# Kernel tuning notes

Measured on AMD Instinct MI355X. Metric: run time of the kernel, lower is better.

Reference implementation:

```python
import jax, jax.numpy as jnp
import numpy as np

WS = (7, 7, 7)          # window size (d, h, w)
N = WS[0] * WS[1] * WS[2]   # 343 tokens per window
C = 96                  # embed_dim
H = 24                  # num_heads  (constraint: embed_dim = 4 * num_heads)
HD = C // H             # head_dim = 4
B = 32                  # number of windows in the batch
SCALE = HD ** -0.5
EPS = 1e-5


def _relative_position_index():
    # identical to the torch buffer construction in MSA_block.__init__
    coords = np.stack(np.meshgrid(np.arange(WS[0]), np.arange(WS[1]), np.arange(WS[2]), indexing='ij'))
    flat = coords.reshape(3, -1)                       # [3, N]
    rel = flat[:, :, None] - flat[:, None, :]          # [3, N, N]
    rel = rel.transpose(1, 2, 0).astype(np.int64)      # [N, N, 3]
    rel[..., 0] += WS[0] - 1
    rel[..., 1] += WS[1] - 1
    rel[..., 2] += WS[2] - 1
    rel[..., 0] *= (2 * WS[1] - 1) * (2 * WS[2] - 1)
    rel[..., 1] *= 2 * WS[2] - 1
    return rel.sum(-1).astype(np.int32)                # [N, N]


def setup_inputs() -> dict:
    key = jax.random.key(0)
    ks = jax.random.split(key, 9)
    table_size = (2 * WS[0] - 1) * (2 * WS[1] - 1) * (2 * WS[2] - 1)   # 2197
    return {
        'x1': jax.random.normal(ks[0], (B, N, C), jnp.float32),
        'x2': jax.random.normal(ks[1], (B, N, C), jnp.float32),
        'qkv_w': jax.random.normal(ks[2], (3 * C, C), jnp.float32) * 0.02,
        'qkv_b': jax.random.normal(ks[3], (3 * C,), jnp.float32) * 0.02,
        'proj_w': jax.random.normal(ks[4], (C, C), jnp.float32) * 0.02,
        'proj_b': jax.random.normal(ks[5], (C,), jnp.float32) * 0.02,
        'rpb_table': jax.random.normal(ks[6], (table_size, H), jnp.float32) * 0.02,
        'fuse_w': jax.random.normal(ks[7], (H, 2 * H), jnp.float32) * 0.1,   # Conv2d 1x1: [out_c=H, in_c=2H]
        'fuse_b': jax.random.normal(ks[8], (H,), jnp.float32) * 0.02,
        'rel_index': jnp.asarray(_relative_position_index()),
    }


def _qkv(x, qkv_w, qkv_b):
    b, n, c = x.shape
    qkv = (x @ qkv_w.T + qkv_b).reshape(b, n, 3, H, HD)
    qkv = jnp.transpose(qkv, (2, 0, 3, 1, 4))          # [3, b, H, n, hd]
    return qkv[0], qkv[1], qkv[2]


def reference(x1, x2, qkv_w, qkv_b, proj_w, proj_b, rpb_table, fuse_w, fuse_b, rel_index):
    b, n, c = x1.shape
    q1, k1, v1 = _qkv(x1, qkv_w, qkv_b)
    q2, k2, v2 = _qkv(x2, qkv_w, qkv_b)
    attn1 = jnp.einsum('bhqd,bhkd->bhqk', q1 * SCALE, k1)
    attn2 = jnp.einsum('bhqd,bhkd->bhqk', q2 * SCALE, k2)

    # fuse: 1x1 Conv2d over channel dim (2H -> H) + InstanceNorm2d + ReLU + Sigmoid
    v = jnp.concatenate((v1, v2), axis=1)              # [b, 2H, n, hd]
    v = jnp.einsum('bcnd,oc->bond', v, fuse_w) + fuse_b[None, :, None, None]
    mean = v.mean(axis=(2, 3), keepdims=True)
    var = v.var(axis=(2, 3), keepdims=True)
    v = (v - mean) * jax.lax.rsqrt(var + EPS)
    v = jax.nn.sigmoid(jax.nn.relu(v))                 # [b, H, n, hd]

    # gathered relative-position bias: [n, n, H] -> [H, n, n]
    bias = rpb_table[rel_index.reshape(-1)].reshape(n, n, H)
    bias = jnp.transpose(bias, (2, 0, 1))

    attn = jax.nn.softmax(attn1 + attn2 + bias[None], axis=-1)
    out = jnp.einsum('bhqk,bhkd->bhqd', attn, v)       # [b, H, n, hd]
    out = jnp.transpose(out, (0, 2, 1, 3)).reshape(b, n, c)
    return out @ proj_w.T + proj_b
```

## Files before the change

### kernel.cpp

```cpp
#include <hip/hip_runtime.h>
#include <hip/hip_bf16.h>

#define N_TOK 343
#define N_PAD 344
#define BT_J 352
#define C_DIM 96
#define H_HEADS 24
#define HD 4
#define B_WIN 32
#define LOG2E 1.4426950408889634f
#define SCALE_Q (0.5f * LOG2E)
#define EPS_IN 1e-5f
#define CH_STR (HD * N_PAD)
#define F4_STR (N_PAD)
#define AP ((size_t)B_WIN * H_HEADS * CH_STR)
#define BT_ELEMS ((size_t)H_HEADS * BT_J * N_PAD)
#define BT_FLOAT_SPACE ((BT_ELEMS + 1) / 2)
#define PS_HALF ((size_t)B_WIN * H_HEADS * N_PAD)

typedef float v2f __attribute__((ext_vector_type(2)));
#define FMA2(a, b, c) __builtin_elementwise_fma(a, b, c)

__device__ __forceinline__ unsigned short f2bf(float v) {
    unsigned u = __float_as_uint(v);
    u += 0x7FFFu + ((u >> 16) & 1u);
    return (unsigned short)(u >> 16);
}

__global__ __launch_bounds__(192) void prep_kernel(const float* __restrict__ x1,
                                                   const float* __restrict__ x2,
                                                   const float* __restrict__ w,
                                                   const float* __restrict__ bqkv,
                                                   const float* __restrict__ rpb,
                                                   const int* __restrict__ rel,
                                                   float* __restrict__ ws,
                                                   unsigned short* __restrict__ bT) {
    __shared__ float smem[12704];
    const int bid = blockIdx.x, tid = threadIdx.x;
    if (bid < 2112) {
        const int r0t = bid % 11;
        const int rest = bid / 11;
        const int sy = rest % 6, b = rest / 6;
        const int s = sy >> 1, src = sy & 1;
        const int r0 = r0t * 32;
        const int rows = min(32, N_TOK - r0);
        float* xs = smem;
        float* wt = smem + 3104;
        for (int e = tid; e < 96 * 96; e += 192) {
            int j = e / 96, k = e - j * 96;
            wt[k * 100 + j] = w[s * 96 * 96 + e];
        }
        const float* xp = (src == 0 ? x1 : x2) + ((size_t)b * N_TOK + r0) * C_DIM;
        for (int e = tid; e < rows * 96; e += 192) {
            int r = e / 96, k = e - r * 96;
            xs[r * 97 + k] = xp[e];
        }
        __syncthreads();
        const int rg = tid & 7, og = tid >> 3;
        const int oc0 = og * 4, rr = rg * 4;
        float acc[4][4];
        #pragma unroll
        for (int i = 0; i < 4; ++i) {
            float bv = bqkv[s * 96 + oc0 + i];
            #pragma unroll
            for (int j = 0; j < 4; ++j) acc[i][j] = bv;
        }
        for (int k = 0; k < 96; ++k) {
            float4 w4 = *(const float4*)&wt[k * 100 + oc0];
            float wv[4] = {w4.x, w4.y, w4.z, w4.w};
            float xv[4];
            #pragma unroll
            for (int j = 0; j < 4; ++j) xv[j] = xs[(rr + j) * 97 + k];
            #pragma unroll
            for (int i = 0; i < 4; ++i)
                #pragma unroll
                for (int j = 0; j < 4; ++j) acc[i][j] += xv[j] * wv[i];
        }
        const float scl = (s == 0) ? SCALE_Q : 1.0f;
        const int slot = (s == 0) ? (src ? 2 : 0) : (s == 1) ? (src ? 3 : 1) : (src ? 5 : 4);
        #pragma unroll
        for (int j = 0; j < 4; ++j) {
            int row = r0 + rr + j;
            if (row > N_TOK) continue;
            size_t base = (((size_t)b * H_HEADS + og) * N_PAD + row) * 4;
            float4 val = (row == N_TOK)
                ? make_float4(0.f, 0.f, 0.f, 0.f)
                : make_float4(acc[0][j] * scl, acc[1][j] * scl,
                              acc[2][j] * scl, acc[3][j] * scl);
            *(float4*)(ws + (size_t)slot * AP + base) = val;
        }
    } else {
        const int bid2 = bid - 2112;
        const int h = bid2 / 121;
        const int t = bid2 - h * 121;
        const int ti = t / 11, tj = t - ti * 11;
        const int i0 = ti * 32, j0 = tj * 32;
        float* tile = smem;
        for (int e = tid; e < 1024; e += 192) {
            int r = e >> 5, c = e & 31;
            int i = i0 + r, j = j0 + c;
            float v = -16384.f;
            if (i < N_TOK && j < N_TOK) v = rpb[rel[i * N_TOK + j] * H_HEADS + h] * LOG2E;
            tile[r * 33 + c] = v;
        }
        __syncthreads();
        for (int e = tid; e < 1024; e += 192) {
            int c = e >> 5, r = e & 31;
            int i = i0 + r, j = j0 + c;
            if (i < N_PAD)
                bT[((size_t)h * BT_J + j) * N_PAD + i] = f2bf(tile[r * 33 + c]);
        }
    }
}

__global__ __launch_bounds__(256) void fuse_kernel(const float* __restrict__ v1,
                                                   const float* __restrict__ v2,
                                                   const float* __restrict__ fw,
                                                   const float* __restrict__ fb,
                                                   float* __restrict__ vf) {
    const int o = blockIdx.x, b = blockIdx.y;
    __shared__ float4 ts4[343];
    __shared__ float red[32];
    __shared__ float fwl[48];
    if (threadIdx.x < 48) fwl[threadIdx.x] = fw[o * 48 + threadIdx.x];
    __syncthreads();
    const float bo = fb[o];
    const float4* p1 = (const float4*)(v1 + (size_t)b * H_HEADS * CH_STR);
    const float4* p2 = (const float4*)(v2 + (size_t)b * H_HEADS * CH_STR);
    float lsum = 0.f, lsq = 0.f;
    for (int e = threadIdx.x; e < 343; e += blockDim.x) {
        float4 acc = make_float4(bo, bo, bo, bo);
        #pragma unroll
        for (int c = 0; c < H_HEADS; ++c) {
            float4 u1 = p1[(size_t)c * F4_STR + e];
            float4 u2 = p2[(size_t)c * F4_STR + e];
            float w1 = fwl[c], w2 = fwl[24 + c];
            acc.x += w1 * u1.x + w2 * u2.x;
            acc.y += w1 * u1.y + w2 * u2.y;
            acc.z += w1 * u1.z + w2 * u2.z;
            acc.w += w1 * u1.w + w2 * u2.w;
        }
        ts4[e] = acc;
        lsum += acc.x + acc.y + acc.z + acc.w;
        lsq += acc.x * acc.x + acc.y * acc.y + acc.z * acc.z + acc.w * acc.w;
    }
    for (int off = 32; off; off >>= 1) {
        lsum += __shfl_xor(lsum, off);
        lsq  += __shfl_xor(lsq, off);
    }
    int wid = threadIdx.x >> 6, lane = threadIdx.x & 63;
    if (lane == 0) { red[wid] = lsum; red[8 + wid] = lsq; }
    __syncthreads();
    if (threadIdx.x == 0) {
        float su = red[0] + red[1] + red[2] + red[3];
        float q  = red[8] + red[9] + red[10] + red[11];
        float mean = su / (float)(N_TOK * HD);
        float var  = q / (float)(N_TOK * HD) - mean * mean;
        red[16] = mean;
        red[17] = rsqrtf(var + EPS_IN);
    }
    __syncthreads();
    const float mean = red[16], inv = red[17];
    float4* outp = (float4*)(vf + ((size_t)b * H_HEADS + o) * CH_STR);
    for (int e = threadIdx.x; e < 343; e += blockDim.x) {
        float4 x = ts4[e];
        float4 r;
        r.x = 1.f / (1.f + __expf(-fmaxf((x.x - mean) * inv, 0.f)));
        r.y = 1.f / (1.f + __expf(-fmaxf((x.y - mean) * inv, 0.f)));
        r.z = 1.f / (1.f + __expf(-fmaxf((x.z - mean) * inv, 0.f)));
        r.w = 1.f / (1.f + __expf(-fmaxf((x.w - mean) * inv, 0.f)));
        outp[e] = r;
    }
}

struct JBatch { unsigned bu[4]; float4 k1[4], k2[4], vv[4]; };

#define LOAD_BATCH(B_, j0_)                                                  \
    _Pragma("unroll")                                                        \
    for (int u = 0; u < 4; ++u) {                                            \
        B_.bu[u] = *(const unsigned*)(bP + (size_t)((j0_) + u) * N_PAD);     \
        B_.k1[u] = K1[(j0_) + u];                                            \
        B_.k2[u] = K2[(j0_) + u];                                            \
        B_.vv[u] = Vv[(j0_) + u];                                            \
    }

#define COMP_BATCH(B_)                                                       \
    _Pragma("unroll")                                                        \
    for (int u = 0; u < 4; ++u) {                                            \
        const float4 k1 = B_.k1[u], k2 = B_.k2[u], v = B_.vv[u];             \
        v2f s2 = {__uint_as_float(B_.bu[u] << 16),                           \
                  __uint_as_float(B_.bu[u] & 0xffff0000u)};                  \
        s2 = FMA2((v2f)(k1.x), q1p0, s2); s2 = FMA2((v2f)(k1.y), q1p1, s2);  \
        s2 = FMA2((v2f)(k1.z), q1p2, s2); s2 = FMA2((v2f)(k1.w), q1p3, s2);  \
        s2 = FMA2((v2f)(k2.x), q2p0, s2); s2 = FMA2((v2f)(k2.y), q2p1, s2);  \
        s2 = FMA2((v2f)(k2.z), q2p2, s2); s2 = FMA2((v2f)(k2.w), q2p3, s2);  \
        const v2f p2 = {exp2f(s2.x), exp2f(s2.y)};                           \
        sum2 += p2;                                                          \
        a0 = FMA2(p2, (v2f)(v.x), a0); a1 = FMA2(p2, (v2f)(v.y), a1);        \
        a2 = FMA2(p2, (v2f)(v.z), a2); a3 = FMA2(p2, (v2f)(v.w), a3);        \
    }

#define ATTN_SETUP                                                                 \
    const size_t off = ((size_t)b * H_HEADS + h) * CH_STR;                         \
    const float4* __restrict__ K1 = (const float4*)(ws + 1 * AP + off);            \
    const float4* __restrict__ K2 = (const float4*)(ws + 3 * AP + off);            \
    const float4* __restrict__ Vv = (const float4*)(vf + off);                     \
    const float*  __restrict__ Q1 = ws + 0 * AP + off;                             \
    const float*  __restrict__ Q2 = ws + 2 * AP + off;                             \
    const int rA = l * 2, rB = rA + 1;                                             \
    const float4 q1a = *(const float4*)&Q1[rA * 4];                                \
    const float4 q1b = *(const float4*)&Q1[rB * 4];                                \
    const float4 q2a = *(const float4*)&Q2[rA * 4];                                \
    const float4 q2b = *(const float4*)&Q2[rB * 4];                                \
    const v2f q1p0 = {q1a.x, q1b.x}, q1p1 = {q1a.y, q1b.y},                        \
              q1p2 = {q1a.z, q1b.z}, q1p3 = {q1a.w, q1b.w};                        \
    const v2f q2p0 = {q2a.x, q2b.x}, q2p1 = {q2a.y, q2b.y},                        \
              q2p2 = {q2a.z, q2b.z}, q2p3 = {q2a.w, q2b.w};                        \
    v2f sum2 = {0.f, 0.f};                                                         \
    v2f a0 = {0.f, 0.f}, a1 = {0.f, 0.f}, a2 = {0.f, 0.f}, a3 = {0.f, 0.f};

template <int NBATCH>
__global__ __launch_bounds__(192) void attn_part_t(const float* __restrict__ ws,
                                                   const unsigned short* __restrict__ bT,
                                                   const float* __restrict__ vf,
                                                   float* __restrict__ Pa,
                                                   float* __restrict__ Ps) {
    const int h = blockIdx.x, b = blockIdx.y, part = blockIdx.z;
    const int l = threadIdx.x;
    if (l >= 172) return;
    ATTN_SETUP
    const int j0h = part * (NBATCH * 8);
    const unsigned short* bP = bT + ((size_t)h * BT_J + j0h) * N_PAD + rA;
    K1 += j0h; K2 += j0h; Vv += j0h;
    JBatch A, B;
    LOAD_BATCH(A, 0)
    LOAD_BATCH(B, 4)
    #pragma unroll
    for (int t = 0; t < NBATCH; ++t) {
        const int jb = t * 8;
        COMP_BATCH(A)
        if (t < NBATCH - 1) { LOAD_BATCH(A, jb + 8) }
        COMP_BATCH(B)
        if (t < NBATCH - 1) { LOAD_BATCH(B, jb + 12) }
    }
    float* PaH = Pa + (size_t)part * AP;
    float* PsH = Ps + (size_t)part * PS_HALF;
    const size_t pi = ((size_t)b * H_HEADS + h) * N_PAD;
    *(float4*)(PaH + (pi + rA) * 4) = make_float4(a0.x, a1.x, a2.x, a3.x);
    *(float4*)(PaH + (pi + rB) * 4) = make_float4(a0.y, a1.y, a2.y, a3.y);
    PsH[pi + rA] = sum2.x;
    PsH[pi + rB] = sum2.y;
}

__global__ __launch_bounds__(192) void attn_full(const float* __restrict__ ws,
                                                 const unsigned short* __restrict__ bT,
                                                 const float* __restrict__ vf,
                                                 float* __restrict__ ao) {
    const int h = blockIdx.x, b = blockIdx.y;
    const int l = threadIdx.x;
    if (l >= 172) return;
    ATTN_SETUP
    const unsigned short* bP = bT + (size_t)h * BT_J * N_PAD + rA;
    JBatch A, B;
    LOAD_BATCH(A, 0)
    LOAD_BATCH(B, 4)
    #pragma unroll
    for (int t = 0; t < 43; ++t) {
        const int jb = t * 8;
        COMP_BATCH(A)
        if (t < 42) { LOAD_BATCH(A, jb + 8) }
        COMP_BATCH(B)
        if (t < 42) { LOAD_BATCH(B, jb + 12) }
    }
    {
        const float inv = 1.f / sum2.x;
        float* op = ao + ((size_t)b * N_TOK + rA) * C_DIM + h * HD;
        *(float4*)op = make_float4(a0.x * inv, a1.x * inv, a2.x * inv, a3.x * inv);
    }
    if (rB < N_TOK) {
        const float inv = 1.f / sum2.y;
        float* op = ao + ((size_t)b * N_TOK + rB) * C_DIM + h * HD;
        *(float4*)op = make_float4(a0.y * inv, a1.y * inv, a2.y * inv, a3.y * inv);
    }
}

__global__ __launch_bounds__(256) void attn_kernel_g(const float* __restrict__ ws,
                                                     const float* __restrict__ rpb,
                                                     const int* __restrict__ rel,
                                                     const float* __restrict__ vf,
                                                     float* __restrict__ ao) {
    const int h = blockIdx.x, b = blockIdx.y;
    __shared__ float k1s[BT_J * 4], k2s[BT_J * 4], vs[BT_J * 4];
    __shared__ float q1s[N_PAD * 4], q2s[N_PAD * 4];
    const size_t off = ((size_t)b * H_HEADS + h) * CH_STR;
    const float* Q1 = ws + 0 * AP + off;
    const float* K1 = ws + 1 * AP + off;
    const float* Q2 = ws + 2 * AP + off;
    const float* K2 = ws + 3 * AP + off;
    const float* V  = vf + off;
    const int tid = threadIdx.x;
    for (int e = tid; e < N_PAD * 4; e += 256) {
        k1s[e] = K1[e]; k2s[e] = K2[e]; vs[e] = V[e];
        q1s[e] = Q1[e]; q2s[e] = Q2[e];
    }
    for (int e = N_PAD * 4 + tid; e < BT_J * 4; e += 256) {
        k1s[e] = 0.f; k2s[e] = 0.f; vs[e] = 0.f;
    }
    __syncthreads();
    const int wid = tid >> 6, lane = tid & 63;
    const int grp = lane >> 4, l16 = lane & 15;
    const float* rpbh = rpb + h;
    for (int t = 0; t < 22; ++t) {
        const int i = t * 16 + wid * 4 + grp;
        const int ig = min(i, N_TOK - 1);
        const float4 q1 = *(const float4*)&q1s[ig * 4];
        const float4 q2 = *(const float4*)&q2s[ig * 4];
        const int* relRow = rel + (size_t)ig * N_TOK;
        float sum = 0.f, a0 = 0.f, a1 = 0.f, a2 = 0.f, a3 = 0.f;
        #pragma unroll 4
        for (int it = 0; it < 22; ++it) {
            const int jj = it * 16 + l16;
            float s = (jj < N_TOK) ? rpbh[relRow[jj] * H_HEADS] * LOG2E : -16384.f;
            const float4 k1 = *(const float4*)&k1s[jj * 4];
            const float4 k2 = *(const float4*)&k2s[jj * 4];
            s = fmaf(q1.x, k1.x, s); s = fmaf(q1.y, k1.y, s);
            s = fmaf(q1.z, k1.z, s); s = fmaf(q1.w, k1.w, s);
            s = fmaf(q2.x, k2.x, s); s = fmaf(q2.y, k2.y, s);
            s = fmaf(q2.z, k2.z, s); s = fmaf(q2.w, k2.w, s);
            const float p = exp2f(s);
            const float4 v = *(const float4*)&vs[jj * 4];
            sum += p;
            a0 = fmaf(p, v.x, a0); a1 = fmaf(p, v.y, a1);
            a2 = fmaf(p, v.z, a2); a3 = fmaf(p, v.w, a3);
        }
        #pragma unroll
        for (int o = 8; o; o >>= 1) {
            sum += __shfl_xor(sum, o, 16);
            a0 += __shfl_xor(a0, o, 16); a1 += __shfl_xor(a1, o, 16);
            a2 += __shfl_xor(a2, o, 16); a3 += __shfl_xor(a3, o, 16);
        }
        if (l16 == 0 && i < N_TOK) {
            const float inv = 1.f / sum;
            float* op = ao + ((size_t)b * N_TOK + i) * C_DIM + h * HD;
            *(float4*)op = make_float4(a0 * inv, a1 * inv, a2 * inv, a3 * inv);
        }
    }
}

__global__ __launch_bounds__(192) void proj_kernel(const float* __restrict__ ao,
                                                   const float* __restrict__ Pa,
                                                   const float* __restrict__ Ps,
                                                   const float* __restrict__ pw,
                                                   const float* __restrict__ pb,
                                                   float* __restrict__ out,
                                                   int split) {
    __shared__ float xs[32 * 97];
    __shared__ float wt[96 * 100];
    __shared__ float sinv[32 * 24];
    const int b = blockIdx.y, row0 = blockIdx.x * 32;
    const int rows = min(32, N_TOK - row0);
    const int tid = threadIdx.x;
    for (int e = tid; e < 96 * 96; e += 192) {
        int c = e / 96, k = e - c * 96;
        wt[k * 100 + c] = pw[e];
    }
    if (split) {
        for (int e = tid; e < rows * 24; e += 192) {
            int r = e / 24, h = e - r * 24;
            size_t pi = ((size_t)b * H_HEADS + h) * N_PAD + row0 + r;
            float s = 0.f;
            for (int p = 0; p < split; ++p) s += Ps[(size_t)p * PS_HALF + pi];
            sinv[r * 24 + h] = 1.f / s;
        }
        __syncthreads();
        for (int e = tid; e < rows * 96; e += 192) {
            int r = e / 96, c = e - r * 96;
            int h = c >> 2, d = c & 3;
            size_t pi = ((size_t)b * H_HEADS + h) * N_PAD + row0 + r;
            float num = 0.f;
            for (int p = 0; p < split; ++p) num += Pa[(size_t)p * AP + pi * 4 + d];
            xs[r * 97 + c] = num * sinv[r * 24 + h];
        }
    } else {
        for (int e = tid; e < rows * 96; e += 192) {
            int r = e / 96, c = e - r * 96;
            xs[r * 97 + c] = ao[((size_t)b * N_TOK + row0) * C_DIM + e];
        }
    }
    __syncthreads();
    const int rg = tid & 7, og = tid >> 3;
    const int oc0 = og * 4, rr = rg * 4;
    float acc[4][4];
    #pragma unroll
    for (int i = 0; i < 4; ++i) {
        float bv = pb[oc0 + i];
        #pragma unroll
        for (int j = 0; j < 4; ++j) acc[i][j] = bv;
    }
    for (int k = 0; k < 96; ++k) {
        float4 w4 = *(const float4*)&wt[k * 100 + oc0];
        float wv[4] = {w4.x, w4.y, w4.z, w4.w};
        float xv[4];
        #pragma unroll
        for (int j = 0; j < 4; ++j) xv[j] = xs[(rr + j) * 97 + k];
        #pragma unroll
        for (int i = 0; i < 4; ++i)
            #pragma unroll
            for (int j = 0; j < 4; ++j) acc[i][j] += xv[j] * wv[i];
    }
    #pragma unroll
    for (int j = 0; j < 4; ++j) {
        int row = row0 + rr + j;
        if (row >= N_TOK) continue;
        *(float4*)(out + ((size_t)b * N_TOK + row) * C_DIM + oc0) =
            make_float4(acc[0][j], acc[1][j], acc[2][j], acc[3][j]);
    }
}

static const void* find_by_size(void* const* d_in, const int* in_sizes, int n_in,
                                int want, int occurrence) {
    int seen = 0;
    for (int i = 0; i < n_in; ++i) {
        if (in_sizes[i] == want) {
            if (seen == occurrence) return d_in[i];
            ++seen;
        }
    }
    return nullptr;
}

extern "C" void kernel_launch(void* const* d_in, const int* in_sizes, int n_in,
                              void* d_out, int out_size, void* d_ws, size_t ws_size,
                              hipStream_t stream) {
    const float* x1     = (const float*)find_by_size(d_in, in_sizes, n_in, 1053696, 0);
    const float* x2     = (const float*)find_by_size(d_in, in_sizes, n_in, 1053696, 1);
    const float* qkv_w  = (const float*)find_by_size(d_in, in_sizes, n_in, 27648, 0);
    const float* qkv_b  = (const float*)find_by_size(d_in, in_sizes, n_in, 288, 0);
    const float* proj_w = (const float*)find_by_size(d_in, in_sizes, n_in, 9216, 0);
    const float* proj_b = (const float*)find_by_size(d_in, in_sizes, n_in, 96, 0);
    const float* rpb    = (const float*)find_by_size(d_in, in_sizes, n_in, 52728, 0);
    const float* fuse_w = (const float*)find_by_size(d_in, in_sizes, n_in, 1152, 0);
    const float* fuse_b = (const float*)find_by_size(d_in, in_sizes, n_in, 24, 0);
    const int*   rel    = (const int*)  find_by_size(d_in, in_sizes, n_in, 117649, 0);

    if (!x1 || !x2 || !qkv_w || !qkv_b || !proj_w || !proj_b || !rpb || !fuse_w ||
        !fuse_b || !rel) {
        x1     = (const float*)d_in[0];
        x2     = (const float*)d_in[1];
        qkv_w  = (const float*)d_in[2];
        qkv_b  = (const float*)d_in[3];
        proj_w = (const float*)d_in[4];
        proj_b = (const float*)d_in[5];
        rpb    = (const float*)d_in[6];
        fuse_w = (const float*)d_in[7];
        fuse_b = (const float*)d_in[8];
        rel    = (const int*)d_in[9];
    }

    float* ws = (float*)d_ws;
    float* V1 = ws + 4 * AP;
    float* V2 = ws + 5 * AP;
    float* VF = ws + 6 * AP;
    float* AO = V1;
    unsigned short* BT = (unsigned short*)(ws + 7 * AP);
    float* PA = ws + 7 * AP + BT_FLOAT_SPACE;
    float* PS4 = PA + 4 * AP;
    float* PS2 = PA + 2 * AP;
    float* out = (float*)d_out;

    const bool use_bias = ws_size >= (7 * AP + BT_FLOAT_SPACE) * sizeof(float);
    const bool split4   = ws_size >= (7 * AP + BT_FLOAT_SPACE + 4 * AP + 4 * PS_HALF) * sizeof(float);
    const bool split2   = ws_size >= (7 * AP + BT_FLOAT_SPACE + 2 * AP + 2 * PS_HALF) * sizeof(float);

    prep_kernel<<<use_bias ? 5016 : 2112, 192, 0, stream>>>(x1, x2, qkv_w, qkv_b,
                                                            rpb, rel, ws, BT);
    fuse_kernel<<<dim3(H_HEADS, B_WIN), 256, 0, stream>>>(V1, V2, fuse_w, fuse_b, VF);
    if (use_bias && split4) {
        attn_part_t<11><<<dim3(H_HEADS, B_WIN, 4), 192, 0, stream>>>(ws, BT, VF, PA, PS4);
        proj_kernel<<<dim3(11, B_WIN), 192, 0, stream>>>(nullptr, PA, PS4, proj_w, proj_b, out, 4);
    } else if (use_bias && split2) {
        attn_part_t<22><<<dim3(H_HEADS, B_WIN, 2), 192, 0, stream>>>(ws, BT, VF, PA, PS2);
        proj_kernel<<<dim3(11, B_WIN), 192, 0, stream>>>(nullptr, PA, PS2, proj_w, proj_b, out, 2);
    } else {
        if (use_bias)
            attn_full<<<dim3(H_HEADS, B_WIN), 192, 0, stream>>>(ws, BT, VF, AO);
        else
            attn_kernel_g<<<dim3(H_HEADS, B_WIN), 256, 0, stream>>>(ws, rpb, rel, VF, AO);
        proj_kernel<<<dim3(11, B_WIN), 192, 0, stream>>>(AO, nullptr, nullptr, proj_w, proj_b, out, 0);
    }
}
```

Before: 158.2 us.

## Transpose GEMM activation tiles, batch heads in bias gather, pair fuse channels

The QKV and projection GEMM tiles now store activations transposed in shared memory, so each k-step reads four rows with one float4 load instead of four scalar loads. Padding rows are zero-filled to keep those vector reads valid. The bias-table build now processes all 24 heads per tile, reading each rel index once and doing coalesced rpb row reads, which cuts the bias-block count from 2904 to 242. The fuse kernel computes two output channels per block, so each v1/v2 load is reused twice, at the cost of more registers and shared memory per block.

Measured after the change: 177.3 us. 1.12x slower.

```diff
diff --git a/kernel.cpp b/kernel.cpp
--- a/kernel.cpp
+++ b/kernel.cpp
@@ -35,7 +35,7 @@
                                                    const int* __restrict__ rel,
                                                    float* __restrict__ ws,
                                                    unsigned short* __restrict__ bT) {
-    __shared__ float smem[12704];
+    __shared__ float smem[13824];
     const int bid = blockIdx.x, tid = threadIdx.x;
     if (bid < 2112) {
         const int r0t = bid % 11;
@@ -44,8 +44,8 @@
         const int s = sy >> 1, src = sy & 1;
         const int r0 = r0t * 32;
         const int rows = min(32, N_TOK - r0);
-        float* xs = smem;
-        float* wt = smem + 3104;
+        float* wt  = smem;
+        float* xsT = smem + 9600;
         for (int e = tid; e < 96 * 96; e += 192) {
             int j = e / 96, k = e - j * 96;
             wt[k * 100 + j] = w[s * 96 * 96 + e];
@@ -53,7 +53,13 @@
         const float* xp = (src == 0 ? x1 : x2) + ((size_t)b * N_TOK + r0) * C_DIM;
         for (int e = tid; e < rows * 96; e += 192) {
             int r = e / 96, k = e - r * 96;
-            xs[r * 97 + k] = xp[e];
+            xsT[k * 44 + r] = xp[e];
+        }
+        if (rows < 32) {
+            for (int e = tid; e < 96 * (32 - rows); e += 192) {
+                int k = e / (32 - rows), r = rows + e % (32 - rows);
+                xsT[k * 44 + r] = 0.f;
+            }
         }
         __syncthreads();
         const int rg = tid & 7, og = tid >> 3;
@@ -67,10 +73,9 @@
         }
         for (int k = 0; k < 96; ++k) {
             float4 w4 = *(const float4*)&wt[k * 100 + oc0];
+            float4 x4 = *(const float4*)&xsT[k * 44 + rr];
             float wv[4] = {w4.x, w4.y, w4.z, w4.w};
-            float xv[4];
-            #pragma unroll
-            for (int j = 0; j < 4; ++j) xv[j] = xs[(rr + j) * 97 + k];
+            float xv[4] = {x4.x, x4.y, x4.z, x4.w};
             #pragma unroll
             for (int i = 0; i < 4; ++i)
                 #pragma unroll
@@ -91,24 +96,29 @@
         }
     } else {
         const int bid2 = bid - 2112;
-        const int h = bid2 / 121;
-        const int t = bid2 - h * 121;
-        const int ti = t / 11, tj = t - ti * 11;
-        const int i0 = ti * 32, j0 = tj * 32;
-        float* tile = smem;
-        for (int e = tid; e < 1024; e += 192) {
-            int r = e >> 5, c = e & 31;
+        const int ti = bid2 / 22, tj = bid2 - ti * 22;
+        const int i0 = ti * 32, j0 = tj * 16;
+        int* srel = (int*)smem;
+        unsigned short* btile = (unsigned short*)(smem + 512);
+        for (int e = tid; e < 512; e += 192) {
+            int r = e >> 4, c = e & 15;
             int i = i0 + r, j = j0 + c;
-            float v = -16384.f;
-            if (i < N_TOK && j < N_TOK) v = rpb[rel[i * N_TOK + j] * H_HEADS + h] * LOG2E;
-            tile[r * 33 + c] = v;
+            srel[e] = (i < N_TOK && j < N_TOK) ? rel[i * N_TOK + j] : -1;
         }
         __syncthreads();
-        for (int e = tid; e < 1024; e += 192) {
-            int c = e >> 5, r = e & 31;
+        for (int e = tid; e < 512 * 24; e += 192) {
+            int ij = e / 24, h = e - (e / 24) * 24;
+            int c = ij >> 5, r = ij & 31;
+            int idx = srel[r * 16 + c];
+            float v = (idx >= 0) ? rpb[idx * 24 + h] * LOG2E : -16384.f;
+            btile[ij * 24 + h] = f2bf(v);
+        }
+        __syncthreads();
+        for (int e = tid; e < 24 * 16 * 32; e += 192) {
+            int r = e & 31, c = (e >> 5) & 15, h = e >> 9;
             int i = i0 + r, j = j0 + c;
             if (i < N_PAD)
-                bT[((size_t)h * BT_J + j) * N_PAD + i] = f2bf(tile[r * 33 + c]);
+                bT[((size_t)h * BT_J + j) * N_PAD + i] = btile[(c * 32 + r) * 24 + h];
         }
     }
 }
@@ -118,58 +128,75 @@
                                                    const float* __restrict__ fw,
                                                    const float* __restrict__ fb,
                                                    float* __restrict__ vf) {
-    const int o = blockIdx.x, b = blockIdx.y;
-    __shared__ float4 ts4[343];
+    const int o1 = blockIdx.x * 2, o2 = o1 + 1, b = blockIdx.y;
+    __shared__ float4 ts4a[343], ts4b[343];
     __shared__ float red[32];
-    __shared__ float fwl[48];
-    if (threadIdx.x < 48) fwl[threadIdx.x] = fw[o * 48 + threadIdx.x];
+    __shared__ float fwl[96];
+    if (threadIdx.x < 48) fwl[threadIdx.x] = fw[o1 * 48 + threadIdx.x];
+    else if (threadIdx.x < 96) fwl[threadIdx.x] = fw[o2 * 48 + threadIdx.x - 48];
     __syncthreads();
-    const float bo = fb[o];
+    const float bo1 = fb[o1], bo2 = fb[o2];
     const float4* p1 = (const float4*)(v1 + (size_t)b * H_HEADS * CH_STR);
     const float4* p2 = (const float4*)(v2 + (size_t)b * H_HEADS * CH_STR);
-    float lsum = 0.f, lsq = 0.f;
+    float ls1 = 0.f, lq1 = 0.f, ls2 = 0.f, lq2 = 0.f;
     for (int e = threadIdx.x; e < 343; e += blockDim.x) {
-        float4 acc = make_float4(bo, bo, bo, bo);
+        float4 a1 = make_float4(bo1, bo1, bo1, bo1);
+        float4 a2 = make_float4(bo2, bo2, bo2, bo2);
         #pragma unroll
         for (int c = 0; c < H_HEADS; ++c) {
             float4 u1 = p1[(size_t)c * F4_STR + e];
             float4 u2 = p2[(size_t)c * F4_STR + e];
-            float w1 = fwl[c], w2 = fwl[24 + c];
-            acc.x += w1 * u1.x + w2 * u2.x;
-            acc.y += w1 * u1.y + w2 * u2.y;
-            acc.z += w1 * u1.z + w2 * u2.z;
-            acc.w += w1 * u1.w + w2 * u2.w;
-        }
-        ts4[e] = acc;
-        lsum += acc.x + acc.y + acc.z + acc.w;
-        lsq += acc.x * acc.x + acc.y * acc.y + acc.z * acc.z + acc.w * acc.w;
+            float w1a = fwl[c], w2a = fwl[24 + c];
+            float w1b = fwl[48 + c], w2b = fwl[72 + c];
+            a1.x += w1a * u1.x + w2a * u2.x; a1.y += w1a * u1.y + w2a * u2.y;
+            a1.z += w1a * u1.z + w2a * u2.z; a1.w += w1a * u1.w + w2a * u2.w;
+            a2.x += w1b * u1.x + w2b * u2.x; a2.y += w1b * u1.y + w2b * u2.y;
+            a2.z += w1b * u1.z + w2b * u2.z; a2.w += w1b * u1.w + w2b * u2.w;
+        }
+        ts4a[e] = a1; ts4b[e] = a2;
+        ls1 += a1.x + a1.y + a1.z + a1.w;
+        lq1 += a1.x * a1.x + a1.y * a1.y + a1.z * a1.z + a1.w * a1.w;
+        ls2 += a2.x + a2.y + a2.z + a2.w;
+        lq2 += a2.x * a2.x + a2.y * a2.y + a2.z * a2.z + a2.w * a2.w;
     }
     for (int off = 32; off; off >>= 1) {
-        lsum += __shfl_xor(lsum, off);
-        lsq  += __shfl_xor(lsq, off);
+        ls1 += __shfl_xor(ls1, off); lq1 += __shfl_xor(lq1, off);
+        ls2 += __shfl_xor(ls2, off); lq2 += __shfl_xor(lq2, off);
     }
     int wid = threadIdx.x >> 6, lane = threadIdx.x & 63;
-    if (lane == 0) { red[wid] = lsum; red[8 + wid] = lsq; }
+    if (lane == 0) {
+        red[wid] = ls1; red[4 + wid] = lq1;
+        red[8 + wid] = ls2; red[12 + wid] = lq2;
+    }
     __syncthreads();
     if (threadIdx.x == 0) {
-        float su = red[0] + red[1] + red[2] + red[3];
-        float q  = red[8] + red[9] + red[10] + red[11];
-        float mean = su / (float)(N_TOK * HD);
-        float var  = q / (float)(N_TOK * HD) - mean * mean;
-        red[16] = mean;
-        red[17] = rsqrtf(var + EPS_IN);
+        const float n = (float)(N_TOK * HD);
+        float s1 = red[0] + red[1] + red[2] + red[3];
+        float q1 = red[4] + red[5] + red[6] + red[7];
+        float s2 = red[8] + red[9] + red[10] + red[11];
+        float q2 = red[12] + red[13] + red[14] + red[15];
+        float m1 = s1 / n, m2 = s2 / n;
+        red[16] = m1; red[17] = rsqrtf(q1 / n - m1 * m1 + EPS_IN);
+        red[18] = m2; red[19] = rsqrtf(q2 / n - m2 * m2 + EPS_IN);
     }
     __syncthreads();
-    const float mean = red[16], inv = red[17];
-    float4* outp = (float4*)(vf + ((size_t)b * H_HEADS + o) * CH_STR);
+    const float m1 = red[16], i1 = red[17], m2 = red[18], i2 = red[19];
+    float4* out1 = (float4*)(vf + ((size_t)b * H_HEADS + o1) * CH_STR);
+    float4* out2 = (float4*)(vf + ((size_t)b * H_HEADS + o2) * CH_STR);
     for (int e = threadIdx.x; e < 343; e += blockDim.x) {
-        float4 x = ts4[e];
+        float4 x = ts4a[e];
         float4 r;
-        r.x = 1.f / (1.f + __expf(-fmaxf((x.x - mean) * inv, 0.f)));
-        r.y = 1.f / (1.f + __expf(-fmaxf((x.y - mean) * inv, 0.f)));
-        r.z = 1.f / (1.f + __expf(-fmaxf((x.z - mean) * inv, 0.f)));
-        r.w = 1.f / (1.f + __expf(-fmaxf((x.w - mean) * inv, 0.f)));
-        outp[e] = r;
+        r.x = 1.f / (1.f + __expf(-fmaxf((x.x - m1) * i1, 0.f)));
+        r.y = 1.f / (1.f + __expf(-fmaxf((x.y - m1) * i1, 0.f)));
+        r.z = 1.f / (1.f + __expf(-fmaxf((x.z - m1) * i1, 0.f)));
+        r.w = 1.f / (1.f + __expf(-fmaxf((x.w - m1) * i1, 0.f)));
+        out1[e] = r;
+        x = ts4b[e];
+        r.x = 1.f / (1.f + __expf(-fmaxf((x.x - m2) * i2, 0.f)));
+        r.y = 1.f / (1.f + __expf(-fmaxf((x.y - m2) * i2, 0.f)));
+        r.z = 1.f / (1.f + __expf(-fmaxf((x.z - m2) * i2, 0.f)));
+        r.w = 1.f / (1.f + __expf(-fmaxf((x.w - m2) * i2, 0.f)));
+        out2[e] = r;
     }
 }
 
@@ -354,7 +381,7 @@
                                                    const float* __restrict__ pb,
                                                    float* __restrict__ out,
                                                    int split) {
-    __shared__ float xs[32 * 97];
+    __shared__ float xsT[96 * 36];
     __shared__ float wt[96 * 100];
     __shared__ float sinv[32 * 24];
     const int b = blockIdx.y, row0 = blockIdx.x * 32;
@@ -364,6 +391,12 @@
         int c = e / 96, k = e - c * 96;
         wt[k * 100 + c] = pw[e];
     }
+    if (rows < 32) {
+        for (int e = tid; e < 96 * (32 - rows); e += 192) {
+            int c = e / (32 - rows), r = rows + e % (32 - rows);
+            xsT[c * 36 + r] = 0.f;
+        }
+    }
     if (split) {
         for (int e = tid; e < rows * 24; e += 192) {
             int r = e / 24, h = e - r * 24;
@@ -379,12 +412,12 @@
             size_t pi = ((size_t)b * H_HEADS + h) * N_PAD + row0 + r;
             float num = 0.f;
             for (int p = 0; p < split; ++p) num += Pa[(size_t)p * AP + pi * 4 + d];
-            xs[r * 97 + c] = num * sinv[r * 24 + h];
+            xsT[c * 36 + r] = num * sinv[r * 24 + h];
         }
     } else {
         for (int e = tid; e < rows * 96; e += 192) {
             int r = e / 96, c = e - r * 96;
-            xs[r * 97 + c] = ao[((size_t)b * N_TOK + row0) * C_DIM + e];
+            xsT[c * 36 + r] = ao[((size_t)b * N_TOK + row0) * C_DIM + e];
         }
     }
     __syncthreads();
@@ -399,10 +432,9 @@
     }
     for (int k = 0; k < 96; ++k) {
         float4 w4 = *(const float4*)&wt[k * 100 + oc0];
+        float4 x4 = *(const float4*)&xsT[k * 36 + rr];
         float wv[4] = {w4.x, w4.y, w4.z, w4.w};
-        float xv[4];
-        #pragma unroll
-        for (int j = 0; j < 4; ++j) xv[j] = xs[(rr + j) * 97 + k];
+        float xv[4] = {x4.x, x4.y, x4.z, x4.w};
         #pragma unroll
         for (int i = 0; i < 4; ++i)
             #pragma unroll
@@ -472,9 +504,9 @@
     const bool split4   = ws_size >= (7 * AP + BT_FLOAT_SPACE + 4 * AP + 4 * PS_HALF) * sizeof(float);
     const bool split2   = ws_size >= (7 * AP + BT_FLOAT_SPACE + 2 * AP + 2 * PS_HALF) * sizeof(float);
 
-    prep_kernel<<<use_bias ? 5016 : 2112, 192, 0, stream>>>(x1, x2, qkv_w, qkv_b,
+    prep_kernel<<<use_bias ? 2354 : 2112, 192, 0, stream>>>(x1, x2, qkv_w, qkv_b,
                                                             rpb, rel, ws, BT);
-    fuse_kernel<<<dim3(H_HEADS, B_WIN), 256, 0, stream>>>(V1, V2, fuse_w, fuse_b, VF);
+    fuse_kernel<<<dim3(12, B_WIN), 256, 0, stream>>>(V1, V2, fuse_w, fuse_b, VF);
     if (use_bias && split4) {
         attn_part_t<11><<<dim3(H_HEADS, B_WIN, 4), 192, 0, stream>>>(ws, BT, VF, PA, PS4);
         proj_kernel<<<dim3(11, B_WIN), 192, 0, stream>>>(nullptr, PA, PS4, proj_w, proj_b, out, 4);
```
